# Kernel tuning notes

Measured on AMD Instinct MI355X. Metric: run time of the kernel, lower is better.

The kernel has to match this reference:

```python
import jax, jax.numpy as jnp
import numpy as np

N, E, C_IN, H, K = 16384, 524288, 128, 64, 64


def setup_inputs() -> dict:
    key = jax.random.key(0)
    ks = jax.random.split(key, 6)
    x = jax.random.normal(ks[0], (N, C_IN), dtype=jnp.float32)
    edge_index = jax.random.randint(ks[1], (2, E), 0, N, dtype=jnp.int32)
    edge_weight = jax.random.uniform(ks[2], (E,), dtype=jnp.float32)
    sc = lambda f: 1.0 / np.sqrt(f)
    # GCNConv lin (no bias inside lin; separate bias), Glorot-ish init
    W1 = jax.random.normal(ks[3], (C_IN, H), dtype=jnp.float32) * sc(C_IN)
    b1 = jnp.zeros((H,), jnp.float32)
    # DMoNPooling MLP: Linear(H,H) then Linear(H,K), no activation between (act=None)
    Wm1 = jax.random.normal(ks[4], (H, H), dtype=jnp.float32) * sc(H)
    bm1 = jnp.zeros((H,), jnp.float32)
    Wm2 = jax.random.normal(ks[5], (H, K), dtype=jnp.float32) * sc(H)
    bm2 = jnp.zeros((K,), jnp.float32)
    return dict(x=x, edge_index=edge_index, edge_weight=edge_weight,
                W1=W1, b1=b1, Wm1=Wm1, bm1=bm1, Wm2=Wm2, bm2=bm2)


def gcn_conv(x, edge_index, edge_weight, W, b, n):
    # GCNConv: add self-loops (weight 1), symmetric deg^-1/2 normalization,
    # aggregate messages from source (row) into target (col).
    row, col = edge_index[0], edge_index[1]
    loop = jnp.arange(n, dtype=edge_index.dtype)
    row = jnp.concatenate([row, loop])
    col = jnp.concatenate([col, loop])
    w = jnp.concatenate([edge_weight, jnp.ones((n,), edge_weight.dtype)])
    deg = jax.ops.segment_sum(w, col, num_segments=n)
    dis = jnp.where(deg > 0, jax.lax.rsqrt(deg), 0.0)
    norm = dis[row] * w * dis[col]
    xw = x @ W  # [N, H]
    out = jax.ops.segment_sum(xw[row] * norm[:, None], col, num_segments=n)
    return out + b


def dmon_pool(h, adj, Wm1, bm1, Wm2, bm2):
    # eval mode: dropout disabled
    s = jax.nn.softmax((h @ Wm1 + bm1) @ Wm2 + bm2, axis=-1)  # [N, K]
    k = s.shape[-1]
    out_adj = s.T @ (adj @ s)  # [K, K]

    # Spectral (modularity) loss; degrees = einsum('ijk->ik', adj) = column sums
    deg = adj.sum(axis=0)  # [N]
    m = deg.sum() / 2
    ca = s.T @ deg  # [K], equals degrees^T s as well (symmetric roles)
    normalizer = jnp.outer(ca, ca) / 2 / m
    spectral_loss = -jnp.trace(out_adj - normalizer) / 2 / m

    # Orthogonality loss
    ss = s.T @ s  # [K, K]
    ss_fro = jnp.sqrt(jnp.sum(ss * ss))
    i_fro = jnp.sqrt(jnp.float32(k))  # ||I_K||_F
    diff = ss / ss_fro - jnp.eye(k, dtype=ss.dtype) / i_fro
    ortho_loss = jnp.sqrt(jnp.sum(diff * diff))

    # Cluster size loss
    cluster_size = s.sum(axis=0)  # [K]
    cluster_loss = jnp.sqrt(jnp.sum(cluster_size * cluster_size)) / h.shape[0] * i_fro - 1.0

    return s, spectral_loss, ortho_loss, cluster_loss


def reference(x, edge_index, edge_weight, W1, b1, Wm1, bm1, Wm2, bm2):
    h = jax.nn.relu(gcn_conv(x, edge_index, edge_weight, W1, b1, N))
    # to_dense_adj(edge_index): dense [N, N], duplicate edges summed
    adj = jnp.zeros((N, N), h.dtype).at[edge_index[0], edge_index[1]].add(1.0)
    s, spec, ortho, clus = dmon_pool(h, adj, Wm1, bm1, Wm2, bm2)
    return s[None], spec + ortho + clus
```

## Files before the change

kernel.cpp:

```cpp
#include <hip/hip_runtime.h>
#include <hip/hip_bf16.h>

typedef float          f4  __attribute__((ext_vector_type(4)));
typedef unsigned short us4 __attribute__((ext_vector_type(4)));
typedef int            i2  __attribute__((ext_vector_type(2)));

template <typename T>
__device__ __forceinline__ T ntload(const T* p) { return __builtin_nontemporal_load(p); }

__device__ __forceinline__ unsigned short f2bf(float f) {
    unsigned u = __float_as_uint(f);
    return (unsigned short)((u + 0x7FFF + ((u >> 16) & 1)) >> 16);
}
__device__ __forceinline__ float bf2f(unsigned short h) {
    return __uint_as_float((unsigned)h << 16);
}

__global__ __launch_bounds__(256) void k_degxw(const int* __restrict__ ei,
                      const float* __restrict__ ew,
                      unsigned* __restrict__ deg_rep,
                      const float* __restrict__ x, const float* __restrict__ W1,
                      float* __restrict__ xw, unsigned short* __restrict__ xw16,
                      int N, int E) {
    __shared__ float w1l[128 * 64];
    __shared__ f4    xt[16][32];
    if (blockIdx.x < 2048) {
        int e = blockIdx.x * 256 + threadIdx.x;
        if (e < E) {
            int c = ntload(ei + E + e);
            float w = ntload(ew + e);
            unsigned q = __float2uint_rn(w * 524288.f);
            atomicAdd(&deg_rep[(size_t)(blockIdx.x & 7) * N + c], (1u << 25) | q);
        }
        return;
    }
    int xbid = blockIdx.x - 2048;
    for (int t = threadIdx.x; t < 128 * 64; t += 256) w1l[t] = W1[t];
    int lane = threadIdx.x & 63;
    int wv   = threadIdx.x >> 6;
    for (int base = xbid * 16; base < N; base += 512 * 16) {
        __syncthreads();
        for (int t = threadIdx.x; t < 16 * 32; t += 256)
            ((f4*)xt)[t] = ntload((const f4*)x + (size_t)base * 32 + t);
        __syncthreads();
        int r0 = wv * 4;
        float a0 = 0.f, a1 = 0.f, a2 = 0.f, a3 = 0.f;
#pragma unroll
        for (int q = 0; q < 32; ++q) {
            f4 x0 = xt[r0][q], x1 = xt[r0 + 1][q], x2 = xt[r0 + 2][q], x3 = xt[r0 + 3][q];
            float wa = w1l[(4 * q + 0) * 64 + lane];
            float wb = w1l[(4 * q + 1) * 64 + lane];
            float wc = w1l[(4 * q + 2) * 64 + lane];
            float wd = w1l[(4 * q + 3) * 64 + lane];
            a0 = fmaf(x0.x, wa, a0); a0 = fmaf(x0.y, wb, a0); a0 = fmaf(x0.z, wc, a0); a0 = fmaf(x0.w, wd, a0);
            a1 = fmaf(x1.x, wa, a1); a1 = fmaf(x1.y, wb, a1); a1 = fmaf(x1.z, wc, a1); a1 = fmaf(x1.w, wd, a1);
            a2 = fmaf(x2.x, wa, a2); a2 = fmaf(x2.y, wb, a2); a2 = fmaf(x2.z, wc, a2); a2 = fmaf(x2.w, wd, a2);
            a3 = fmaf(x3.x, wa, a3); a3 = fmaf(x3.y, wb, a3); a3 = fmaf(x3.z, wc, a3); a3 = fmaf(x3.w, wd, a3);
        }
        int gr = base + r0;
        __builtin_nontemporal_store(a0, xw + (size_t)(gr + 0) * 64 + lane);
        __builtin_nontemporal_store(a1, xw + (size_t)(gr + 1) * 64 + lane);
        __builtin_nontemporal_store(a2, xw + (size_t)(gr + 2) * 64 + lane);
        __builtin_nontemporal_store(a3, xw + (size_t)(gr + 3) * 64 + lane);
        xw16[(size_t)(gr + 0) * 64 + lane] = f2bf(a0);
        xw16[(size_t)(gr + 1) * 64 + lane] = f2bf(a1);
        xw16[(size_t)(gr + 2) * 64 + lane] = f2bf(a2);
        xw16[(size_t)(gr + 3) * 64 + lane] = f2bf(a3);
    }
}

__global__ void k_red(const unsigned* __restrict__ deg_rep,
                      int* __restrict__ cursor_rep, int* __restrict__ cnt,
                      float* __restrict__ dis, int N) {
    int c = blockIdx.x * blockDim.x + threadIdx.x;
    if (c >= N) return;
    int run = 0;
    unsigned wsum = 0;
#pragma unroll
    for (int rep = 0; rep < 8; ++rep) {
        unsigned p = deg_rep[(size_t)rep * N + c];
        cursor_rep[(size_t)rep * N + c] = run;
        run += (int)(p >> 25);
        wsum += (p & ((1u << 25) - 1));
    }
    cnt[c] = run;
    dis[c] = rsqrtf((float)wsum * (1.f / 524288.f) + 1.0f);
}

__global__ void k_scan(const int* __restrict__ cnt, int* __restrict__ offs, int N) {
    __shared__ int wsum[16];
    int tid = threadIdx.x;
    int lane = tid & 63, wv = tid >> 6;
    int base = tid * 16;
    int loc[16];
    int sum = 0;
#pragma unroll
    for (int i = 0; i < 16; ++i) { loc[i] = sum; sum += cnt[base + i]; }
    int s = sum;
#pragma unroll
    for (int o = 1; o < 64; o <<= 1) {
        int t = __shfl_up(s, o);
        if (lane >= o) s += t;
    }
    if (lane == 63) wsum[wv] = s;
    __syncthreads();
    if (wv == 0 && lane < 16) {
        int ws = wsum[lane];
        int ss = ws;
#pragma unroll
        for (int o = 1; o < 16; o <<= 1) {
            int t = __shfl_up(ss, o);
            if (lane >= o) ss += t;
        }
        wsum[lane] = ss - ws;
    }
    __syncthreads();
    int excl = s - sum + wsum[wv];
#pragma unroll
    for (int i = 0; i < 16; ++i) offs[base + i] = excl + loc[i];
    if (tid == 1023) offs[N] = excl + sum;
}

__global__ void k_bucket(const int* __restrict__ ei, const float* __restrict__ ew,
                         const float* __restrict__ dis, const int* __restrict__ offs,
                         int* __restrict__ cursor_rep, i2* __restrict__ barr,
                         int N, int E) {
    int e = blockIdx.x * blockDim.x + threadIdx.x;
    if (e < E) {
        int rep = blockIdx.x & 7;
        int r = ntload(ei + e), c = ntload(ei + E + e);
        float norm = dis[r] * ntload(ew + e) * dis[c];
        int pos = offs[c] + atomicAdd(&cursor_rep[(size_t)rep * N + c], 1);
        i2 rec; rec.x = r; rec.y = __float_as_int(norm);
        barr[pos] = rec;
    }
}

__global__ __launch_bounds__(512) void k_gmlp(const int* __restrict__ offs,
                         const i2* __restrict__ barr,
                         const float* __restrict__ xw, const unsigned short* __restrict__ xw16,
                         const float* __restrict__ dis, const float* __restrict__ b1,
                         const float* __restrict__ Wm1, const float* __restrict__ bm1,
                         const float* __restrict__ Wm2, const float* __restrict__ bm2,
                         float* __restrict__ s, unsigned short* __restrict__ s16, int N) {
    __shared__ float w1m[4096], w2m[4096];
    __shared__ float hsc[8][2][64];
    __shared__ float tsc[8][2][64];
    for (int t = threadIdx.x; t < 4096; t += 512) { w1m[t] = Wm1[t]; w2m[t] = Wm2[t]; }
    __syncthreads();
    int lane = threadIdx.x & 63;
    int sub = lane >> 4, q = lane & 15;
    int wv   = threadIdx.x >> 6;
    int NP   = N >> 1;
    int nw   = 8 * gridDim.x;
    int cp   = blockIdx.x * 8 + wv;
    if (cp >= NP) return;
    int c0 = 2 * cp, c1 = c0 + 1;
    int beg = ntload(offs + c0), mid = ntload(offs + c1), end = ntload(offs + c1 + 1);
    i2 bcur = (beg + lane < end) ? ntload(barr + beg + lane) : (i2){0, 0};
    const us4* xw16v = (const us4*)xw16;
    for (;;) {
        f4 A0 = {0.f, 0.f, 0.f, 0.f}, A1 = A0, B0 = A0, B1 = A0;
        int i = beg;
        while (i < end) {
            int inext = i + 64;
            i2 bnxt = {0, 0};
            if (inext + lane < end) bnxt = ntload(barr + inext + lane);
            int nloc = min(64, end - i);
            int   rv = bcur.x;
            float nv = __int_as_float(bcur.y);
            int jmax = (nloc + 3) >> 2;
            int j = 0;
            for (; j + 4 <= jmax; j += 4) {
                int e0 = 4 * j + sub;
                int g0 = i + e0;
                int   r0 = __shfl(rv, e0),      r1 = __shfl(rv, e0 + 4);
                int   r2 = __shfl(rv, e0 + 8),  r3 = __shfl(rv, e0 + 12);
                float n0 = __shfl(nv, e0),      n1 = __shfl(nv, e0 + 4);
                float n2 = __shfl(nv, e0 + 8),  n3 = __shfl(nv, e0 + 12);
                us4 u0 = xw16v[(size_t)r0 * 16 + q];
                us4 u1 = xw16v[(size_t)r1 * 16 + q];
                us4 u2 = xw16v[(size_t)r2 * 16 + q];
                us4 u3 = xw16v[(size_t)r3 * 16 + q];
                float a0w = (g0      < mid) ? n0 : 0.f, b0w = n0 - a0w;
                float a1w = (g0 + 4  < mid) ? n1 : 0.f, b1w = n1 - a1w;
                float a2w = (g0 + 8  < mid) ? n2 : 0.f, b2w = n2 - a2w;
                float a3w = (g0 + 12 < mid) ? n3 : 0.f, b3w = n3 - a3w;
                A0.x = fmaf(bf2f(u0.x), a0w, A0.x); A0.y = fmaf(bf2f(u0.y), a0w, A0.y);
                A0.z = fmaf(bf2f(u0.z), a0w, A0.z); A0.w = fmaf(bf2f(u0.w), a0w, A0.w);
                B0.x = fmaf(bf2f(u0.x), b0w, B0.x); B0.y = fmaf(bf2f(u0.y), b0w, B0.y);
                B0.z = fmaf(bf2f(u0.z), b0w, B0.z); B0.w = fmaf(bf2f(u0.w), b0w, B0.w);
                A1.x = fmaf(bf2f(u1.x), a1w, A1.x); A1.y = fmaf(bf2f(u1.y), a1w, A1.y);
                A1.z = fmaf(bf2f(u1.z), a1w, A1.z); A1.w = fmaf(bf2f(u1.w), a1w, A1.w);
                B1.x = fmaf(bf2f(u1.x), b1w, B1.x); B1.y = fmaf(bf2f(u1.y), b1w, B1.y);
                B1.z = fmaf(bf2f(u1.z), b1w, B1.z); B1.w = fmaf(bf2f(u1.w), b1w, B1.w);
                A0.x = fmaf(bf2f(u2.x), a2w, A0.x); A0.y = fmaf(bf2f(u2.y), a2w, A0.y);
                A0.z = fmaf(bf2f(u2.z), a2w, A0.z); A0.w = fmaf(bf2f(u2.w), a2w, A0.w);
                B0.x = fmaf(bf2f(u2.x), b2w, B0.x); B0.y = fmaf(bf2f(u2.y), b2w, B0.y);
                B0.z = fmaf(bf2f(u2.z), b2w, B0.z); B0.w = fmaf(bf2f(u2.w), b2w, B0.w);
                A1.x = fmaf(bf2f(u3.x), a3w, A1.x); A1.y = fmaf(bf2f(u3.y), a3w, A1.y);
                A1.z = fmaf(bf2f(u3.z), a3w, A1.z); A1.w = fmaf(bf2f(u3.w), a3w, A1.w);
                B1.x = fmaf(bf2f(u3.x), b3w, B1.x); B1.y = fmaf(bf2f(u3.y), b3w, B1.y);
                B1.z = fmaf(bf2f(u3.z), b3w, B1.z); B1.w = fmaf(bf2f(u3.w), b3w, B1.w);
            }
            for (; j < jmax; ++j) {
                int e = 4 * j + sub;
                int g = i + e;
                int   r  = __shfl(rv, e);
                float nm = __shfl(nv, e);
                us4 u = xw16v[(size_t)r * 16 + q];
                float aw = (g < mid) ? nm : 0.f, bw = nm - aw;
                A0.x = fmaf(bf2f(u.x), aw, A0.x); A0.y = fmaf(bf2f(u.y), aw, A0.y);
                A0.z = fmaf(bf2f(u.z), aw, A0.z); A0.w = fmaf(bf2f(u.w), aw, A0.w);
                B0.x = fmaf(bf2f(u.x), bw, B0.x); B0.y = fmaf(bf2f(u.y), bw, B0.y);
                B0.z = fmaf(bf2f(u.z), bw, B0.z); B0.w = fmaf(bf2f(u.w), bw, B0.w);
            }
            i = inext;
            bcur = bnxt;
        }
        int cpn = cp + nw;
        int begN = 0, midN = 0, endN = 0;
        if (cpn < NP) {
            begN = ntload(offs + 2 * cpn);
            midN = ntload(offs + 2 * cpn + 1);
            endN = ntload(offs + 2 * cpn + 2);
        }
        A0.x += A1.x; A0.y += A1.y; A0.z += A1.z; A0.w += A1.w;
        B0.x += B1.x; B0.y += B1.y; B0.z += B1.z; B0.w += B1.w;
        A0.x += __shfl_xor(A0.x, 16); A0.y += __shfl_xor(A0.y, 16);
        A0.z += __shfl_xor(A0.z, 16); A0.w += __shfl_xor(A0.w, 16);
        B0.x += __shfl_xor(B0.x, 16); B0.y += __shfl_xor(B0.y, 16);
        B0.z += __shfl_xor(B0.z, 16); B0.w += __shfl_xor(B0.w, 16);
        A0.x += __shfl_xor(A0.x, 32); A0.y += __shfl_xor(A0.y, 32);
        A0.z += __shfl_xor(A0.z, 32); A0.w += __shfl_xor(A0.w, 32);
        B0.x += __shfl_xor(B0.x, 32); B0.y += __shfl_xor(B0.y, 32);
        B0.z += __shfl_xor(B0.z, 32); B0.w += __shfl_xor(B0.w, 32);
        if (cpn < NP) bcur = (begN + lane < endN) ? ntload(barr + begN + lane) : (i2){0, 0};
        f4 bb = ((const f4*)b1)[q];
        f4 self0 = ntload((const f4*)xw + (size_t)c0 * 16 + q);
        f4 self1 = ntload((const f4*)xw + (size_t)c1 * 16 + q);
        float d0 = dis[c0], d1 = dis[c1];
        float dd0 = d0 * d0, dd1 = d1 * d1;
        f4 v0, v1;
        v0.x = A0.x + self0.x * dd0 + bb.x; v0.y = A0.y + self0.y * dd0 + bb.y;
        v0.z = A0.z + self0.z * dd0 + bb.z; v0.w = A0.w + self0.w * dd0 + bb.w;
        v1.x = B0.x + self1.x * dd1 + bb.x; v1.y = B0.y + self1.y * dd1 + bb.y;
        v1.z = B0.z + self1.z * dd1 + bb.z; v1.w = B0.w + self1.w * dd1 + bb.w;
        v0.x = v0.x > 0.f ? v0.x : 0.f; v0.y = v0.y > 0.f ? v0.y : 0.f;
        v0.z = v0.z > 0.f ? v0.z : 0.f; v0.w = v0.w > 0.f ? v0.w : 0.f;
        v1.x = v1.x > 0.f ? v1.x : 0.f; v1.y = v1.y > 0.f ? v1.y : 0.f;
        v1.z = v1.z > 0.f ? v1.z : 0.f; v1.w = v1.w > 0.f ? v1.w : 0.f;
        if (sub == 0) {
            ((f4*)hsc[wv][0])[q] = v0;
            ((f4*)hsc[wv][1])[q] = v1;
        }
        float t0 = bm1[lane], t1 = t0;
#pragma unroll
        for (int k = 0; k < 16; ++k) {
            f4 ha = ((f4*)hsc[wv][0])[k];
            f4 hb = ((f4*)hsc[wv][1])[k];
            float wa = w1m[(4 * k + 0) * 64 + lane];
            float wb = w1m[(4 * k + 1) * 64 + lane];
            float wc = w1m[(4 * k + 2) * 64 + lane];
            float wd = w1m[(4 * k + 3) * 64 + lane];
            t0 = fmaf(ha.x, wa, t0); t0 = fmaf(ha.y, wb, t0);
            t0 = fmaf(ha.z, wc, t0); t0 = fmaf(ha.w, wd, t0);
            t1 = fmaf(hb.x, wa, t1); t1 = fmaf(hb.y, wb, t1);
            t1 = fmaf(hb.z, wc, t1); t1 = fmaf(hb.w, wd, t1);
        }
        tsc[wv][0][lane] = t0;
        tsc[wv][1][lane] = t1;
        float g0 = bm2[lane], g1 = g0;
#pragma unroll
        for (int k = 0; k < 16; ++k) {
            f4 ta = ((f4*)tsc[wv][0])[k];
            f4 tb = ((f4*)tsc[wv][1])[k];
            float wa = w2m[(4 * k + 0) * 64 + lane];
            float wb = w2m[(4 * k + 1) * 64 + lane];
            float wc = w2m[(4 * k + 2) * 64 + lane];
            float wd = w2m[(4 * k + 3) * 64 + lane];
            g0 = fmaf(ta.x, wa, g0); g0 = fmaf(ta.y, wb, g0);
            g0 = fmaf(ta.z, wc, g0); g0 = fmaf(ta.w, wd, g0);
            g1 = fmaf(tb.x, wa, g1); g1 = fmaf(tb.y, wb, g1);
            g1 = fmaf(tb.z, wc, g1); g1 = fmaf(tb.w, wd, g1);
        }
        float m0 = g0, m1 = g1;
#pragma unroll
        for (int o = 32; o > 0; o >>= 1) {
            m0 = fmaxf(m0, __shfl_xor(m0, o));
            m1 = fmaxf(m1, __shfl_xor(m1, o));
        }
        float e0 = __expf(g0 - m0), e1 = __expf(g1 - m1);
        float z0 = e0, z1 = e1;
#pragma unroll
        for (int o = 32; o > 0; o >>= 1) {
            z0 += __shfl_xor(z0, o);
            z1 += __shfl_xor(z1, o);
        }
        float o0 = e0 / z0, o1 = e1 / z1;
        __builtin_nontemporal_store(o0, s + (size_t)c0 * 64 + lane);
        __builtin_nontemporal_store(o1, s + (size_t)c1 * 64 + lane);
        s16[(size_t)c0 * 64 + lane] = f2bf(o0);
        s16[(size_t)c1 * 64 + lane] = f2bf(o1);
        if (cpn >= NP) break;
        cp = cpn; c0 = 2 * cp; c1 = c0 + 1;
        beg = begN; mid = midN; end = endN;
    }
}

__global__ __launch_bounds__(256) void k_rt(const int* __restrict__ offs,
                         const i2* __restrict__ barr,
                         const unsigned short* __restrict__ s16,
                         const float* __restrict__ s, const int* __restrict__ cnt,
                         float* __restrict__ ssg, float* __restrict__ cag,
                         float* __restrict__ csg, float* __restrict__ tracearr, int N) {
    __shared__ float tile[64][64];
    __shared__ float bsum;
    int lane = threadIdx.x & 63;
    int wv   = threadIdx.x >> 6;
    if (blockIdx.x >= 2048) {
        int base = (blockIdx.x - 2048) * 64;
        if (base >= N) return;
        for (int t = threadIdx.x; t < 1024; t += 256)
            ((f4*)tile)[t] = ntload((const f4*)(s + (size_t)base * 64) + t);
        __syncthreads();
        float acc[16];
#pragma unroll
        for (int i = 0; i < 16; ++i) acc[i] = 0.f;
        for (int r = 0; r < 64; ++r) {
            float sj = tile[r][lane];
            const float* brow = &tile[r][wv * 16];
#pragma unroll
            for (int i = 0; i < 16; ++i) acc[i] = fmaf(brow[i], sj, acc[i]);
        }
        float csj = 0.f, caj = 0.f;
#pragma unroll
        for (int i = 0; i < 16; ++i) {
            int r = wv * 16 + i;
            float sj = tile[r][lane];
            csj += sj;
            caj = fmaf(sj, (float)cnt[base + r], caj);
        }
#pragma unroll
        for (int i = 0; i < 16; ++i) atomicAdd(&ssg[(wv * 16 + i) * 64 + lane], acc[i]);
        atomicAdd(&csg[lane], csj);
        atomicAdd(&cag[lane], caj);
        return;
    }
    int sub = lane >> 4, q = lane & 15;
    int wid  = blockIdx.x * 4 + wv;
    int nw   = 4 * 2048;
    const us4* s16v = (const us4*)s16;
    float tacc = 0.f;
    for (int cp = wid; cp < (N >> 1); cp += nw) {
        int c0 = 2 * cp, c1 = c0 + 1;
        int beg = ntload(offs + c0), mid = ntload(offs + c1), end = ntload(offs + c1 + 1);
        us4 scu0 = s16v[(size_t)c0 * 16 + q];
        us4 scu1 = s16v[(size_t)c1 * 16 + q];
        f4 sc0 = {bf2f(scu0.x), bf2f(scu0.y), bf2f(scu0.z), bf2f(scu0.w)};
        f4 sc1 = {bf2f(scu1.x), bf2f(scu1.y), bf2f(scu1.z), bf2f(scu1.w)};
        f4 A0 = {0.f, 0.f, 0.f, 0.f}, A1 = A0, B0 = A0, B1 = A0;
        int i = beg;
        int rcur = (beg + lane < end) ? ntload(barr + beg + lane).x : 0;
        while (i < end) {
            int inext = i + 64;
            int rnxt = 0;
            if (inext + lane < end) rnxt = ntload(barr + inext + lane).x;
            int nloc = min(64, end - i);
            int rv = rcur;
            int jmax = (nloc + 3) >> 2;
            int j = 0;
            for (; j + 4 <= jmax; j += 4) {
                int e0 = 4 * j + sub;
                int g0 = i + e0;
                int r0 = __shfl(rv, e0),     r1 = __shfl(rv, e0 + 4);
                int r2 = __shfl(rv, e0 + 8), r3 = __shfl(rv, e0 + 12);
                float n0 = (e0      < nloc) ? 1.f : 0.f;
                float n1 = (e0 + 4  < nloc) ? 1.f : 0.f;
                float n2 = (e0 + 8  < nloc) ? 1.f : 0.f;
                float n3 = (e0 + 12 < nloc) ? 1.f : 0.f;
                us4 u0 = s16v[(size_t)r0 * 16 + q];
                us4 u1 = s16v[(size_t)r1 * 16 + q];
                us4 u2 = s16v[(size_t)r2 * 16 + q];
                us4 u3 = s16v[(size_t)r3 * 16 + q];
                float a0w = (g0      < mid) ? n0 : 0.f, b0w = n0 - a0w;
                float a1w = (g0 + 4  < mid) ? n1 : 0.f, b1w = n1 - a1w;
                float a2w = (g0 + 8  < mid) ? n2 : 0.f, b2w = n2 - a2w;
                float a3w = (g0 + 12 < mid) ? n3 : 0.f, b3w = n3 - a3w;
                A0.x = fmaf(bf2f(u0.x), a0w, A0.x); A0.y = fmaf(bf2f(u0.y), a0w, A0.y);
                A0.z = fmaf(bf2f(u0.z), a0w, A0.z); A0.w = fmaf(bf2f(u0.w), a0w, A0.w);
                B0.x = fmaf(bf2f(u0.x), b0w, B0.x); B0.y = fmaf(bf2f(u0.y), b0w, B0.y);
                B0.z = fmaf(bf2f(u0.z), b0w, B0.z); B0.w = fmaf(bf2f(u0.w), b0w, B0.w);
                A1.x = fmaf(bf2f(u1.x), a1w, A1.x); A1.y = fmaf(bf2f(u1.y), a1w, A1.y);
                A1.z = fmaf(bf2f(u1.z), a1w, A1.z); A1.w = fmaf(bf2f(u1.w), a1w, A1.w);
                B1.x = fmaf(bf2f(u1.x), b1w, B1.x); B1.y = fmaf(bf2f(u1.y), b1w, B1.y);
                B1.z = fmaf(bf2f(u1.z), b1w, B1.z); B1.w = fmaf(bf2f(u1.w), b1w, B1.w);
                A0.x = fmaf(bf2f(u2.x), a2w, A0.x); A0.y = fmaf(bf2f(u2.y), a2w, A0.y);
                A0.z = fmaf(bf2f(u2.z), a2w, A0.z); A0.w = fmaf(bf2f(u2.w), a2w, A0.w);
                B0.x = fmaf(bf2f(u2.x), b2w, B0.x); B0.y = fmaf(bf2f(u2.y), b2w, B0.y);
                B0.z = fmaf(bf2f(u2.z), b2w, B0.z); B0.w = fmaf(bf2f(u2.w), b2w, B0.w);
                A1.x = fmaf(bf2f(u3.x), a3w, A1.x); A1.y = fmaf(bf2f(u3.y), a3w, A1.y);
                A1.z = fmaf(bf2f(u3.z), a3w, A1.z); A1.w = fmaf(bf2f(u3.w), a3w, A1.w);
                B1.x = fmaf(bf2f(u3.x), b3w, B1.x); B1.y = fmaf(bf2f(u3.y), b3w, B1.y);
                B1.z = fmaf(bf2f(u3.z), b3w, B1.z); B1.w = fmaf(bf2f(u3.w), b3w, B1.w);
            }
            for (; j < jmax; ++j) {
                int e = 4 * j + sub;
                int g = i + e;
                int r = __shfl(rv, e);
                float m = (e < nloc) ? 1.f : 0.f;
                us4 u = s16v[(size_t)r * 16 + q];
                float aw = (g < mid) ? m : 0.f, bw = m - aw;
                A0.x = fmaf(bf2f(u.x), aw, A0.x); A0.y = fmaf(bf2f(u.y), aw, A0.y);
                A0.z = fmaf(bf2f(u.z), aw, A0.z); A0.w = fmaf(bf2f(u.w), aw, A0.w);
                B0.x = fmaf(bf2f(u.x), bw, B0.x); B0.y = fmaf(bf2f(u.y), bw, B0.y);
                B0.z = fmaf(bf2f(u.z), bw, B0.z); B0.w = fmaf(bf2f(u.w), bw, B0.w);
            }
            i = inext;
            rcur = rnxt;
        }
        A0.x += A1.x; A0.y += A1.y; A0.z += A1.z; A0.w += A1.w;
        B0.x += B1.x; B0.y += B1.y; B0.z += B1.z; B0.w += B1.w;
        A0.x += __shfl_xor(A0.x, 16); A0.y += __shfl_xor(A0.y, 16);
        A0.z += __shfl_xor(A0.z, 16); A0.w += __shfl_xor(A0.w, 16);
        B0.x += __shfl_xor(B0.x, 16); B0.y += __shfl_xor(B0.y, 16);
        B0.z += __shfl_xor(B0.z, 16); B0.w += __shfl_xor(B0.w, 16);
        A0.x += __shfl_xor(A0.x, 32); A0.y += __shfl_xor(A0.y, 32);
        A0.z += __shfl_xor(A0.z, 32); A0.w += __shfl_xor(A0.w, 32);
        B0.x += __shfl_xor(B0.x, 32); B0.y += __shfl_xor(B0.y, 32);
        B0.z += __shfl_xor(B0.z, 32); B0.w += __shfl_xor(B0.w, 32);
        tacc += A0.x * sc0.x + A0.y * sc0.y + A0.z * sc0.z + A0.w * sc0.w;
        tacc += B0.x * sc1.x + B0.y * sc1.y + B0.z * sc1.z + B0.w * sc1.w;
    }
    tacc *= 0.25f;
#pragma unroll
    for (int o = 32; o > 0; o >>= 1) tacc += __shfl_xor(tacc, o);
    if (threadIdx.x == 0) bsum = 0.f;
    __syncthreads();
    if (lane == 0) atomicAdd(&bsum, tacc);
    __syncthreads();
    if (threadIdx.x == 0) tracearr[blockIdx.x] = bsum;
}

__global__ void k_final(const float* __restrict__ ssg, const float* __restrict__ cag,
                        const float* __restrict__ csg, const float* __restrict__ tracearr,
                        int ntr, float Ef, float Nf, float* __restrict__ out) {
    __shared__ float red[256];
    int tid = threadIdx.x;

    float a = 0.f;
    for (int t = tid; t < ntr; t += 256) a += tracearr[t];
    red[tid] = a; __syncthreads();
    for (int o = 128; o > 0; o >>= 1) { if (tid < o) red[tid] += red[tid + o]; __syncthreads(); }
    float trace = red[0]; __syncthreads();

    a = 0.f;
    for (int t = tid; t < 4096; t += 256) { float v = ssg[t]; a += v * v; }
    red[tid] = a; __syncthreads();
    for (int o = 128; o > 0; o >>= 1) { if (tid < o) red[tid] += red[tid + o]; __syncthreads(); }
    float ss_sumsq = red[0]; __syncthreads();

    a = (tid < 64) ? ssg[tid * 64 + tid] : 0.f;
    red[tid] = a; __syncthreads();
    for (int o = 128; o > 0; o >>= 1) { if (tid < o) red[tid] += red[tid + o]; __syncthreads(); }
    float tr_ss = red[0]; __syncthreads();

    a = (tid < 64) ? cag[tid] * cag[tid] : 0.f;
    red[tid] = a; __syncthreads();
    for (int o = 128; o > 0; o >>= 1) { if (tid < o) red[tid] += red[tid + o]; __syncthreads(); }
    float ca_ss = red[0]; __syncthreads();

    a = (tid < 64) ? csg[tid] * csg[tid] : 0.f;
    red[tid] = a; __syncthreads();
    for (int o = 128; o > 0; o >>= 1) { if (tid < o) red[tid] += red[tid + o]; __syncthreads(); }
    float cs_ss = red[0];

    if (tid == 0) {
        float spec = -(trace - ca_ss / Ef) / Ef;
        float ss_fro = sqrtf(ss_sumsq);
        float ortho = sqrtf(fmaxf(2.f - tr_ss / (4.f * ss_fro), 0.f));
        float clus = sqrtf(cs_ss) / Nf * 8.f - 1.f;
        out[0] = spec + ortho + clus;
    }
}

extern "C" void kernel_launch(void* const* d_in, const int* in_sizes, int n_in,
                              void* d_out, int out_size, void* d_ws, size_t ws_size,
                              hipStream_t stream) {
    const float* x   = (const float*)d_in[0];
    const int*   ei  = (const int*)d_in[1];
    const float* ew  = (const float*)d_in[2];
    const float* W1  = (const float*)d_in[3];
    const float* b1  = (const float*)d_in[4];
    const float* Wm1 = (const float*)d_in[5];
    const float* bm1 = (const float*)d_in[6];
    const float* Wm2 = (const float*)d_in[7];
    const float* bm2 = (const float*)d_in[8];

    const int N = in_sizes[0] / 128;
    const int E = in_sizes[2];
    const int TGRID = 2304;

    char* base = (char*)d_ws;
    unsigned* deg_rep = (unsigned*)base;
    float* ssg = (float*)(base + (size_t)32 * N);
    float* cag = ssg + 4096;
    float* csg = cag + 64;
    size_t zbytes = (size_t)32 * N + (4096 + 128) * 4;
    char* up = base + ((zbytes + 15) & ~(size_t)15);
    int*   cursor_rep = (int*)up;     up += (size_t)32 * N;
    int*   cnt = (int*)up;            up += (size_t)4 * N;
    float* dis = (float*)up;          up += (size_t)4 * N;
    int*   offs = (int*)up;           up += (size_t)4 * (N + 1);
    float* tracearr = (float*)up;     up += (size_t)4 * 2048;
    up = (char*)(((size_t)up + 15) & ~(size_t)15);
    float* xw = (float*)up;           up += (size_t)4 * N * 64;
    i2*    barr = (i2*)up;            up += (size_t)8 * E;
    unsigned short* xw16 = (unsigned short*)up; up += (size_t)2 * N * 64;
    unsigned short* s16  = (unsigned short*)up;
    float* sbuf = (float*)d_out;

    hipMemsetAsync(d_ws, 0, zbytes, stream);

    k_degxw<<<2560, 256, 0, stream>>>(ei, ew, deg_rep, x, W1, xw, xw16, N, E);
    k_red<<<(N + 255) / 256, 256, 0, stream>>>(deg_rep, cursor_rep, cnt, dis, N);
    k_scan<<<1, 1024, 0, stream>>>(cnt, offs, N);
    k_bucket<<<(E + 255) / 256, 256, 0, stream>>>(ei, ew, dis, offs, cursor_rep, barr, N, E);
    k_gmlp<<<512, 512, 0, stream>>>(offs, barr, xw, xw16, dis, b1, Wm1, bm1, Wm2, bm2, sbuf, s16, N);
    k_rt<<<TGRID, 256, 0, stream>>>(offs, barr, s16, sbuf, cnt, ssg, cag, csg, tracearr, N);
    k_final<<<1, 256, 0, stream>>>(ssg, cag, csg, tracearr, 2048, (float)E, (float)N,
                                   ((float*)d_out) + (size_t)N * 64);
}
```

Before: 220.0 us.

## Prefetch next column pair in trace kernel, halve its grid, and process two edges per bucket thread

The trace part of k_rt now uses 1024 blocks that loop over column pairs and prefetch the next pair's offsets, s16 rows and first barr chunk while reducing the current pair. This hides gather latency between iterations. k_bucket now handles two edges per thread, half an array apart, so more atomics and loads are in flight per thread. The replica index for degree and cursor atomics is now derived from the edge index, not the block index. Halving the k_rt grid lowers parallelism in exchange for the software pipelining, and the two-edge split assumes E is even.

```diff
diff --git a/kernel.cpp b/kernel.cpp
--- a/kernel.cpp
+++ b/kernel.cpp
@@ -30,7 +30,7 @@
             int c = ntload(ei + E + e);
             float w = ntload(ew + e);
             unsigned q = __float2uint_rn(w * 524288.f);
-            atomicAdd(&deg_rep[(size_t)(blockIdx.x & 7) * N + c], (1u << 25) | q);
+            atomicAdd(&deg_rep[(size_t)((e >> 8) & 7) * N + c], (1u << 25) | q);
         }
         return;
     }
@@ -125,14 +125,22 @@
                          const float* __restrict__ dis, const int* __restrict__ offs,
                          int* __restrict__ cursor_rep, i2* __restrict__ barr,
                          int N, int E) {
-    int e = blockIdx.x * blockDim.x + threadIdx.x;
-    if (e < E) {
-        int rep = blockIdx.x & 7;
-        int r = ntload(ei + e), c = ntload(ei + E + e);
-        float norm = dis[r] * ntload(ew + e) * dis[c];
-        int pos = offs[c] + atomicAdd(&cursor_rep[(size_t)rep * N + c], 1);
-        i2 rec; rec.x = r; rec.y = __float_as_int(norm);
-        barr[pos] = rec;
+    int t = blockIdx.x * blockDim.x + threadIdx.x;
+    int h = E >> 1;
+    if (t < h) {
+        int e0 = t, e1 = t + h;
+        int r0 = ntload(ei + e0), c0 = ntload(ei + E + e0);
+        int r1 = ntload(ei + e1), c1 = ntload(ei + E + e1);
+        float w0 = ntload(ew + e0), w1 = ntload(ew + e1);
+        float n0 = dis[r0] * w0 * dis[c0];
+        float n1 = dis[r1] * w1 * dis[c1];
+        int rep0 = (e0 >> 8) & 7, rep1 = (e1 >> 8) & 7;
+        int p0 = offs[c0] + atomicAdd(&cursor_rep[(size_t)rep0 * N + c0], 1);
+        int p1 = offs[c1] + atomicAdd(&cursor_rep[(size_t)rep1 * N + c1], 1);
+        i2 x0; x0.x = r0; x0.y = __float_as_int(n0);
+        i2 x1; x1.x = r1; x1.y = __float_as_int(n1);
+        barr[p0] = x0;
+        barr[p1] = x1;
     }
 }
 
@@ -318,8 +326,8 @@
     __shared__ float bsum;
     int lane = threadIdx.x & 63;
     int wv   = threadIdx.x >> 6;
-    if (blockIdx.x >= 2048) {
-        int base = (blockIdx.x - 2048) * 64;
+    if (blockIdx.x >= 1024) {
+        int base = (blockIdx.x - 1024) * 64;
         if (base >= N) return;
         for (int t = threadIdx.x; t < 1024; t += 256)
             ((f4*)tile)[t] = ntload((const f4*)(s + (size_t)base * 64) + t);
@@ -348,89 +356,109 @@
         return;
     }
     int sub = lane >> 4, q = lane & 15;
-    int wid  = blockIdx.x * 4 + wv;
-    int nw   = 4 * 2048;
+    int NP = N >> 1;
+    int nw = 4 * 1024;
+    int cp = blockIdx.x * 4 + wv;
     const us4* s16v = (const us4*)s16;
     float tacc = 0.f;
-    for (int cp = wid; cp < (N >> 1); cp += nw) {
+    if (cp < NP) {
         int c0 = 2 * cp, c1 = c0 + 1;
         int beg = ntload(offs + c0), mid = ntload(offs + c1), end = ntload(offs + c1 + 1);
         us4 scu0 = s16v[(size_t)c0 * 16 + q];
         us4 scu1 = s16v[(size_t)c1 * 16 + q];
-        f4 sc0 = {bf2f(scu0.x), bf2f(scu0.y), bf2f(scu0.z), bf2f(scu0.w)};
-        f4 sc1 = {bf2f(scu1.x), bf2f(scu1.y), bf2f(scu1.z), bf2f(scu1.w)};
-        f4 A0 = {0.f, 0.f, 0.f, 0.f}, A1 = A0, B0 = A0, B1 = A0;
-        int i = beg;
         int rcur = (beg + lane < end) ? ntload(barr + beg + lane).x : 0;
-        while (i < end) {
-            int inext = i + 64;
-            int rnxt = 0;
-            if (inext + lane < end) rnxt = ntload(barr + inext + lane).x;
-            int nloc = min(64, end - i);
-            int rv = rcur;
-            int jmax = (nloc + 3) >> 2;
-            int j = 0;
-            for (; j + 4 <= jmax; j += 4) {
-                int e0 = 4 * j + sub;
-                int g0 = i + e0;
-                int r0 = __shfl(rv, e0),     r1 = __shfl(rv, e0 + 4);
-                int r2 = __shfl(rv, e0 + 8), r3 = __shfl(rv, e0 + 12);
-                float n0 = (e0      < nloc) ? 1.f : 0.f;
-                float n1 = (e0 + 4  < nloc) ? 1.f : 0.f;
-                float n2 = (e0 + 8  < nloc) ? 1.f : 0.f;
-                float n3 = (e0 + 12 < nloc) ? 1.f : 0.f;
-                us4 u0 = s16v[(size_t)r0 * 16 + q];
-                us4 u1 = s16v[(size_t)r1 * 16 + q];
-                us4 u2 = s16v[(size_t)r2 * 16 + q];
-                us4 u3 = s16v[(size_t)r3 * 16 + q];
-                float a0w = (g0      < mid) ? n0 : 0.f, b0w = n0 - a0w;
-                float a1w = (g0 + 4  < mid) ? n1 : 0.f, b1w = n1 - a1w;
-                float a2w = (g0 + 8  < mid) ? n2 : 0.f, b2w = n2 - a2w;
-                float a3w = (g0 + 12 < mid) ? n3 : 0.f, b3w = n3 - a3w;
-                A0.x = fmaf(bf2f(u0.x), a0w, A0.x); A0.y = fmaf(bf2f(u0.y), a0w, A0.y);
-                A0.z = fmaf(bf2f(u0.z), a0w, A0.z); A0.w = fmaf(bf2f(u0.w), a0w, A0.w);
-                B0.x = fmaf(bf2f(u0.x), b0w, B0.x); B0.y = fmaf(bf2f(u0.y), b0w, B0.y);
-                B0.z = fmaf(bf2f(u0.z), b0w, B0.z); B0.w = fmaf(bf2f(u0.w), b0w, B0.w);
-                A1.x = fmaf(bf2f(u1.x), a1w, A1.x); A1.y = fmaf(bf2f(u1.y), a1w, A1.y);
-                A1.z = fmaf(bf2f(u1.z), a1w, A1.z); A1.w = fmaf(bf2f(u1.w), a1w, A1.w);
-                B1.x = fmaf(bf2f(u1.x), b1w, B1.x); B1.y = fmaf(bf2f(u1.y), b1w, B1.y);
-                B1.z = fmaf(bf2f(u1.z), b1w, B1.z); B1.w = fmaf(bf2f(u1.w), b1w, B1.w);
-                A0.x = fmaf(bf2f(u2.x), a2w, A0.x); A0.y = fmaf(bf2f(u2.y), a2w, A0.y);
-                A0.z = fmaf(bf2f(u2.z), a2w, A0.z); A0.w = fmaf(bf2f(u2.w), a2w, A0.w);
-                B0.x = fmaf(bf2f(u2.x), b2w, B0.x); B0.y = fmaf(bf2f(u2.y), b2w, B0.y);
-                B0.z = fmaf(bf2f(u2.z), b2w, B0.z); B0.w = fmaf(bf2f(u2.w), b2w, B0.w);
-                A1.x = fmaf(bf2f(u3.x), a3w, A1.x); A1.y = fmaf(bf2f(u3.y), a3w, A1.y);
-                A1.z = fmaf(bf2f(u3.z), a3w, A1.z); A1.w = fmaf(bf2f(u3.w), a3w, A1.w);
-                B1.x = fmaf(bf2f(u3.x), b3w, B1.x); B1.y = fmaf(bf2f(u3.y), b3w, B1.y);
-                B1.z = fmaf(bf2f(u3.z), b3w, B1.z); B1.w = fmaf(bf2f(u3.w), b3w, B1.w);
+        for (;;) {
+            f4 A0 = {0.f, 0.f, 0.f, 0.f}, A1 = A0, B0 = A0, B1 = A0;
+            int i = beg;
+            while (i < end) {
+                int inext = i + 64;
+                int rnxt = 0;
+                if (inext + lane < end) rnxt = ntload(barr + inext + lane).x;
+                int nloc = min(64, end - i);
+                int rv = rcur;
+                int jmax = (nloc + 3) >> 2;
+                int j = 0;
+                for (; j + 4 <= jmax; j += 4) {
+                    int e0 = 4 * j + sub;
+                    int g0 = i + e0;
+                    int r0 = __shfl(rv, e0),     r1 = __shfl(rv, e0 + 4);
+                    int r2 = __shfl(rv, e0 + 8), r3 = __shfl(rv, e0 + 12);
+                    float n0 = (e0      < nloc) ? 1.f : 0.f;
+                    float n1 = (e0 + 4  < nloc) ? 1.f : 0.f;
+                    float n2 = (e0 + 8  < nloc) ? 1.f : 0.f;
+                    float n3 = (e0 + 12 < nloc) ? 1.f : 0.f;
+                    us4 u0 = s16v[(size_t)r0 * 16 + q];
+                    us4 u1 = s16v[(size_t)r1 * 16 + q];
+                    us4 u2 = s16v[(size_t)r2 * 16 + q];
+                    us4 u3 = s16v[(size_t)r3 * 16 + q];
+                    float a0w = (g0      < mid) ? n0 : 0.f, b0w = n0 - a0w;
+                    float a1w = (g0 + 4  < mid) ? n1 : 0.f, b1w = n1 - a1w;
+                    float a2w = (g0 + 8  < mid) ? n2 : 0.f, b2w = n2 - a2w;
+                    float a3w = (g0 + 12 < mid) ? n3 : 0.f, b3w = n3 - a3w;
+                    A0.x = fmaf(bf2f(u0.x), a0w, A0.x); A0.y = fmaf(bf2f(u0.y), a0w, A0.y);
+                    A0.z = fmaf(bf2f(u0.z), a0w, A0.z); A0.w = fmaf(bf2f(u0.w), a0w, A0.w);
+                    B0.x = fmaf(bf2f(u0.x), b0w, B0.x); B0.y = fmaf(bf2f(u0.y), b0w, B0.y);
+                    B0.z = fmaf(bf2f(u0.z), b0w, B0.z); B0.w = fmaf(bf2f(u0.w), b0w, B0.w);
+                    A1.x = fmaf(bf2f(u1.x), a1w, A1.x); A1.y = fmaf(bf2f(u1.y), a1w, A1.y);
+                    A1.z = fmaf(bf2f(u1.z), a1w, A1.z); A1.w = fmaf(bf2f(u1.w), a1w, A1.w);
+                    B1.x = fmaf(bf2f(u1.x), b1w, B1.x); B1.y = fmaf(bf2f(u1.y), b1w, B1.y);
+                    B1.z = fmaf(bf2f(u1.z), b1w, B1.z); B1.w = fmaf(bf2f(u1.w), b1w, B1.w);
+                    A0.x = fmaf(bf2f(u2.x), a2w, A0.x); A0.y = fmaf(bf2f(u2.y), a2w, A0.y);
+                    A0.z = fmaf(bf2f(u2.z), a2w, A0.z); A0.w = fmaf(bf2f(u2.w), a2w, A0.w);
+                    B0.x = fmaf(bf2f(u2.x), b2w, B0.x); B0.y = fmaf(bf2f(u2.y), b2w, B0.y);
+                    B0.z = fmaf(bf2f(u2.z), b2w, B0.z); B0.w = fmaf(bf2f(u2.w), b2w, B0.w);
+                    A1.x = fmaf(bf2f(u3.x), a3w, A1.x); A1.y = fmaf(bf2f(u3.y), a3w, A1.y);
+                    A1.z = fmaf(bf2f(u3.z), a3w, A1.z); A1.w = fmaf(bf2f(u3.w), a3w, A1.w);
+                    B1.x = fmaf(bf2f(u3.x), b3w, B1.x); B1.y = fmaf(bf2f(u3.y), b3w, B1.y);
+                    B1.z = fmaf(bf2f(u3.z), b3w, B1.z); B1.w = fmaf(bf2f(u3.w), b3w, B1.w);
+                }
+                for (; j < jmax; ++j) {
+                    int e = 4 * j + sub;
+                    int g = i + e;
+                    int r = __shfl(rv, e);
+                    float m = (e < nloc) ? 1.f : 0.f;
+                    us4 u = s16v[(size_t)r * 16 + q];
+                    float aw = (g < mid) ? m : 0.f, bw = m - aw;
+                    A0.x = fmaf(bf2f(u.x), aw, A0.x); A0.y = fmaf(bf2f(u.y), aw, A0.y);
+                    A0.z = fmaf(bf2f(u.z), aw, A0.z); A0.w = fmaf(bf2f(u.w), aw, A0.w);
+                    B0.x = fmaf(bf2f(u.x), bw, B0.x); B0.y = fmaf(bf2f(u.y), bw, B0.y);
+                    B0.z = fmaf(bf2f(u.z), bw, B0.z); B0.w = fmaf(bf2f(u.w), bw, B0.w);
+                }
+                i = inext;
+                rcur = rnxt;
             }
-            for (; j < jmax; ++j) {
-                int e = 4 * j + sub;
-                int g = i + e;
-                int r = __shfl(rv, e);
-                float m = (e < nloc) ? 1.f : 0.f;
-                us4 u = s16v[(size_t)r * 16 + q];
-                float aw = (g < mid) ? m : 0.f, bw = m - aw;
-                A0.x = fmaf(bf2f(u.x), aw, A0.x); A0.y = fmaf(bf2f(u.y), aw, A0.y);
-                A0.z = fmaf(bf2f(u.z), aw, A0.z); A0.w = fmaf(bf2f(u.w), aw, A0.w);
-                B0.x = fmaf(bf2f(u.x), bw, B0.x); B0.y = fmaf(bf2f(u.y), bw, B0.y);
-                B0.z = fmaf(bf2f(u.z), bw, B0.z); B0.w = fmaf(bf2f(u.w), bw, B0.w);
+            int cpn = cp + nw;
+            int begN = 0, midN = 0, endN = 0;
+            if (cpn < NP) {
+                begN = ntload(offs + 2 * cpn);
+                midN = ntload(offs + 2 * cpn + 1);
+                endN = ntload(offs + 2 * cpn + 2);
             }
-            i = inext;
-            rcur = rnxt;
-        }
-        A0.x += A1.x; A0.y += A1.y; A0.z += A1.z; A0.w += A1.w;
-        B0.x += B1.x; B0.y += B1.y; B0.z += B1.z; B0.w += B1.w;
-        A0.x += __shfl_xor(A0.x, 16); A0.y += __shfl_xor(A0.y, 16);
-        A0.z += __shfl_xor(A0.z, 16); A0.w += __shfl_xor(A0.w, 16);
-        B0.x += __shfl_xor(B0.x, 16); B0.y += __shfl_xor(B0.y, 16);
-        B0.z += __shfl_xor(B0.z, 16); B0.w += __shfl_xor(B0.w, 16);
-        A0.x += __shfl_xor(A0.x, 32); A0.y += __shfl_xor(A0.y, 32);
-        A0.z += __shfl_xor(A0.z, 32); A0.w += __shfl_xor(A0.w, 32);
-        B0.x += __shfl_xor(B0.x, 32); B0.y += __shfl_xor(B0.y, 32);
-        B0.z += __shfl_xor(B0.z, 32); B0.w += __shfl_xor(B0.w, 32);
-        tacc += A0.x * sc0.x + A0.y * sc0.y + A0.z * sc0.z + A0.w * sc0.w;
-        tacc += B0.x * sc1.x + B0.y * sc1.y + B0.z * sc1.z + B0.w * sc1.w;
+            A0.x += A1.x; A0.y += A1.y; A0.z += A1.z; A0.w += A1.w;
+            B0.x += B1.x; B0.y += B1.y; B0.z += B1.z; B0.w += B1.w;
+            A0.x += __shfl_xor(A0.x, 16); A0.y += __shfl_xor(A0.y, 16);
+            A0.z += __shfl_xor(A0.z, 16); A0.w += __shfl_xor(A0.w, 16);
+            B0.x += __shfl_xor(B0.x, 16); B0.y += __shfl_xor(B0.y, 16);
+            B0.z += __shfl_xor(B0.z, 16); B0.w += __shfl_xor(B0.w, 16);
+            A0.x += __shfl_xor(A0.x, 32); A0.y += __shfl_xor(A0.y, 32);
+            A0.z += __shfl_xor(A0.z, 32); A0.w += __shfl_xor(A0.w, 32);
+            B0.x += __shfl_xor(B0.x, 32); B0.y += __shfl_xor(B0.y, 32);
+            B0.z += __shfl_xor(B0.z, 32); B0.w += __shfl_xor(B0.w, 32);
+            us4 scu0N = {0, 0, 0, 0}, scu1N = {0, 0, 0, 0};
+            if (cpn < NP) {
+                scu0N = s16v[(size_t)(2 * cpn) * 16 + q];
+                scu1N = s16v[(size_t)(2 * cpn + 1) * 16 + q];
+                rcur = (begN + lane < endN) ? ntload(barr + begN + lane).x : 0;
+            }
+            f4 sc0 = {bf2f(scu0.x), bf2f(scu0.y), bf2f(scu0.z), bf2f(scu0.w)};
+            f4 sc1 = {bf2f(scu1.x), bf2f(scu1.y), bf2f(scu1.z), bf2f(scu1.w)};
+            tacc += A0.x * sc0.x + A0.y * sc0.y + A0.z * sc0.z + A0.w * sc0.w;
+            tacc += B0.x * sc1.x + B0.y * sc1.y + B0.z * sc1.z + B0.w * sc1.w;
+            if (cpn >= NP) break;
+            cp = cpn;
+            beg = begN; mid = midN; end = endN;
+            scu0 = scu0N; scu1 = scu1N;
+        }
     }
     tacc *= 0.25f;
 #pragma unroll
@@ -499,7 +527,7 @@
 
     const int N = in_sizes[0] / 128;
     const int E = in_sizes[2];
-    const int TGRID = 2304;
+    const int TGRID = 1280;
 
     char* base = (char*)d_ws;
     unsigned* deg_rep = (unsigned*)base;
@@ -512,7 +540,7 @@
     int*   cnt = (int*)up;            up += (size_t)4 * N;
     float* dis = (float*)up;          up += (size_t)4 * N;
     int*   offs = (int*)up;           up += (size_t)4 * (N + 1);
-    float* tracearr = (float*)up;     up += (size_t)4 * 2048;
+    float* tracearr = (float*)up;     up += (size_t)4 * 1024;
     up = (char*)(((size_t)up + 15) & ~(size_t)15);
     float* xw = (float*)up;           up += (size_t)4 * N * 64;
     i2*    barr = (i2*)up;            up += (size_t)8 * E;
@@ -525,9 +553,9 @@
     k_degxw<<<2560, 256, 0, stream>>>(ei, ew, deg_rep, x, W1, xw, xw16, N, E);
     k_red<<<(N + 255) / 256, 256, 0, stream>>>(deg_rep, cursor_rep, cnt, dis, N);
     k_scan<<<1, 1024, 0, stream>>>(cnt, offs, N);
-    k_bucket<<<(E + 255) / 256, 256, 0, stream>>>(ei, ew, dis, offs, cursor_rep, barr, N, E);
+    k_bucket<<<(E / 2 + 255) / 256, 256, 0, stream>>>(ei, ew, dis, offs, cursor_rep, barr, N, E);
     k_gmlp<<<512, 512, 0, stream>>>(offs, barr, xw, xw16, dis, b1, Wm1, bm1, Wm2, bm2, sbuf, s16, N);
     k_rt<<<TGRID, 256, 0, stream>>>(offs, barr, s16, sbuf, cnt, ssg, cag, csg, tracearr, N);
-    k_final<<<1, 256, 0, stream>>>(ssg, cag, csg, tracearr, 2048, (float)E, (float)N,
+    k_final<<<1, 256, 0, stream>>>(ssg, cag, csg, tracearr, 1024, (float)E, (float)N,
                                    ((float*)d_out) + (size_t)N * 64);
 }
```

Result: faster. 214.6 us, median of 2 (-2.5%).
